# Kernel tuning notes

Hardware: AMD Instinct MI355X
Metric: run time of the kernel (lower is better)

Reference implementation:

```python
import jax, jax.numpy as jnp
import numpy as np


def _log_g(x):
    # log_g(x) = log(relu(x)+1) if x >= 0 else x
    return jnp.where(x >= 0, jnp.log1p(jnp.maximum(x, 0.0)), x)


def _min_gru(hg):
    # hg: [B, H, L] -> [B, H/2, L]
    h, gate = jnp.split(hg, 2, axis=1)
    log_coeffs = -jax.nn.softplus(gate)                    # log(1 - z)
    log_values = -jax.nn.softplus(-gate) + _log_g(h)       # log(z) + log g(h)
    a_star = jnp.cumsum(log_coeffs, axis=2)
    log_h0_plus_b_star = jax.lax.cumlogsumexp(log_values - a_star, axis=2)
    return jnp.exp(a_star + log_h0_plus_b_star)


def setup_inputs() -> dict:
    key = jax.random.key(0)
    B, H, L = 8, 512, 8192
    x = jax.random.normal(key, (B, H, L), dtype=jnp.float32)
    return {"x": x}


def reference(x) -> jnp.ndarray:
    # bidirectional minGRU: forward scan on first half of channels,
    # reversed scan on second half.
    fore, back = jnp.split(x, 2, axis=1)
    out_fore = _min_gru(fore)
    out_back = jnp.flip(_min_gru(jnp.flip(back, axis=2)), axis=2)
    return jnp.concatenate([out_fore, out_back], axis=1)  # [B, H/2, L]
```

## Files before the change

kernel.cpp:

```cpp
#include <hip/hip_runtime.h>
#include <math.h>


#define SEQ_L 8192
#define NTHREADS 256
#define PER_THREAD 8
#define TILE (NTHREADS * PER_THREAD)
#define NTILES (SEQ_L / TILE)

__global__ __launch_bounds__(NTHREADS) void mingru_scan_kernel(
    const float* __restrict__ x, float* __restrict__ out) {
    const int blk = blockIdx.x;
    const int dir = blk >> 10;
    const int s   = blk & 1023;
    const int b   = s >> 7;
    const int c   = s & 127;

    const int tid  = threadIdx.x;
    const int lane = tid & 63;
    const int wave = tid >> 6;

    const float* __restrict__ hrow = x + (size_t)((b * 512) + (dir * 256) + c) * SEQ_L;
    const float* __restrict__ grow = hrow + (size_t)128 * SEQ_L;
    float* __restrict__ orow = out + (size_t)((b * 256) + (dir * 128) + c) * SEQ_L;

    __shared__ float sA[2][4];
    __shared__ float sB[2][4];

    float carry = 0.0f;

    {
    }
    int base0 = tid * PER_THREAD;
    int idx0  = dir ? (SEQ_L - base0 - PER_THREAD) : base0;
    float4 nh0 = *(const float4*)(hrow + idx0);
    float4 nh1 = *(const float4*)(hrow + idx0 + 4);
    float4 ng0 = *(const float4*)(grow + idx0);
    float4 ng1 = *(const float4*)(grow + idx0 + 4);

#pragma unroll
    for (int t = 0; t < NTILES; ++t) {
        const float4 h0 = nh0, h1 = nh1, g0 = ng0, g1 = ng1;

        if (t + 1 < NTILES) {
            const int nb = (t + 1) * TILE + tid * PER_THREAD;
            const int ni = dir ? (SEQ_L - nb - PER_THREAD) : nb;
            nh0 = *(const float4*)(hrow + ni);
            nh1 = *(const float4*)(hrow + ni + 4);
            ng0 = *(const float4*)(grow + ni);
            ng1 = *(const float4*)(grow + ni + 4);
        }

        float hv[PER_THREAD], gv[PER_THREAD];
        if (dir == 0) {
            hv[0]=h0.x; hv[1]=h0.y; hv[2]=h0.z; hv[3]=h0.w;
            hv[4]=h1.x; hv[5]=h1.y; hv[6]=h1.z; hv[7]=h1.w;
            gv[0]=g0.x; gv[1]=g0.y; gv[2]=g0.z; gv[3]=g0.w;
            gv[4]=g1.x; gv[5]=g1.y; gv[6]=g1.z; gv[7]=g1.w;
        } else {
            hv[0]=h1.w; hv[1]=h1.z; hv[2]=h1.y; hv[3]=h1.x;
            hv[4]=h0.w; hv[5]=h0.z; hv[6]=h0.y; hv[7]=h0.x;
            gv[0]=g1.w; gv[1]=g1.z; gv[2]=g1.y; gv[3]=g1.x;
            gv[4]=g0.w; gv[5]=g0.z; gv[6]=g0.y; gv[7]=g0.x;
        }

        float pp[PER_THREAD], ov0[PER_THREAD];
        float ca = 1.0f, cb = 0.0f;
#pragma unroll
        for (int j = 0; j < PER_THREAD; ++j) {
            const float gt = gv[j];
            const float e  = __expf(-fabsf(gt));
            const float r  = 1.0f / (1.0f + e);
            const float sn = e * r;
            const float z  = (gt >= 0.0f) ? r  : sn;
            const float a  = (gt >= 0.0f) ? sn : r;
            const float hh = hv[j];
            const float gf = (hh >= 0.0f) ? (hh + 1.0f) : __expf(hh);
            const float bb = z * gf;
            cb = a * cb + bb;
            ca = a * ca;
            ov0[j] = cb;
            pp[j]  = ca;
        }

        float pa = ca, pb = cb;
#pragma unroll
        for (int d = 1; d < 64; d <<= 1) {
            const float oa = __shfl_up(pa, d);
            const float ob = __shfl_up(pb, d);
            if (lane >= d) {
                pb = pa * ob + pb;
                pa = pa * oa;
            }
        }

        const int buf = t & 1;
        if (lane == 63) { sA[buf][wave] = pa; sB[buf][wave] = pb; }
        __syncthreads();

        float st = carry;
        for (int w = 0; w < wave; ++w) st = sA[buf][w] * st + sB[buf][w];
        float ea = __shfl_up(pa, 1);
        float eb = __shfl_up(pb, 1);
        if (lane == 0) { ea = 1.0f; eb = 0.0f; }
        st = ea * st + eb;

        float ov[PER_THREAD];
#pragma unroll
        for (int j = 0; j < PER_THREAD; ++j) ov[j] = ov0[j] + st * pp[j];

        const int base = t * TILE + tid * PER_THREAD;
        if (dir == 0) {
            *(float4*)(orow + base)     = make_float4(ov[0], ov[1], ov[2], ov[3]);
            *(float4*)(orow + base + 4) = make_float4(ov[4], ov[5], ov[6], ov[7]);
        } else {
            const int p = SEQ_L - base - PER_THREAD;
            *(float4*)(orow + p)     = make_float4(ov[7], ov[6], ov[5], ov[4]);
            *(float4*)(orow + p + 4) = make_float4(ov[3], ov[2], ov[1], ov[0]);
        }

        float nc = carry;
#pragma unroll
        for (int w = 0; w < 4; ++w) nc = sA[buf][w] * nc + sB[buf][w];
        carry = nc;
    }
}

extern "C" void kernel_launch(void* const* d_in, const int* in_sizes, int n_in,
                              void* d_out, int out_size, void* d_ws, size_t ws_size,
                              hipStream_t stream) {
    const float* x = (const float*)d_in[0];
    float* out = (float*)d_out;
    mingru_scan_kernel<<<2048, NTHREADS, 0, stream>>>(x, out);
}
```

Measured before the change: 209.5 us.

## Scan whole row in one pass with 1024-thread blocks and nontemporal memory ops

Each block now uses 1024 threads so a full 8192-element row is handled in a single tile, with no loop over four tiles and no carry chain between them. The cross-wave combine now reads 16 wave aggregates from shared memory using a predicated unrolled loop. Loads and stores become nontemporal vector accesses to avoid polluting cache with streamed data. In exchange, occupancy now depends on register use at 1024 threads per block, and the load prefetching across tiles is gone, so latency is covered only by running many waves at once.

```diff
diff --git a/kernel.cpp b/kernel.cpp
--- a/kernel.cpp
+++ b/kernel.cpp
@@ -3,12 +3,12 @@
 
 
 #define SEQ_L 8192
-#define NTHREADS 256
+#define NTHREADS 1024
 #define PER_THREAD 8
-#define TILE (NTHREADS * PER_THREAD)
-#define NTILES (SEQ_L / TILE)
 
-__global__ __launch_bounds__(NTHREADS) void mingru_scan_kernel(
+typedef float f4 __attribute__((ext_vector_type(4)));
+
+__global__ __launch_bounds__(NTHREADS, 8) void mingru_scan_kernel(
     const float* __restrict__ x, float* __restrict__ out) {
     const int blk = blockIdx.x;
     const int dir = blk >> 10;
@@ -24,105 +24,90 @@
     const float* __restrict__ grow = hrow + (size_t)128 * SEQ_L;
     float* __restrict__ orow = out + (size_t)((b * 256) + (dir * 128) + c) * SEQ_L;
 
-    __shared__ float sA[2][4];
-    __shared__ float sB[2][4];
+    __shared__ float sA[16];
+    __shared__ float sB[16];
 
-    float carry = 0.0f;
+    const int base = tid * PER_THREAD;
+    const int idx  = dir ? (SEQ_L - base - PER_THREAD) : base;
 
-    {
+    const f4 h0 = __builtin_nontemporal_load((const f4*)(hrow + idx));
+    const f4 h1 = __builtin_nontemporal_load((const f4*)(hrow + idx + 4));
+    const f4 g0 = __builtin_nontemporal_load((const f4*)(grow + idx));
+    const f4 g1 = __builtin_nontemporal_load((const f4*)(grow + idx + 4));
+
+    float hv[PER_THREAD], gv[PER_THREAD];
+    if (dir == 0) {
+        hv[0]=h0.x; hv[1]=h0.y; hv[2]=h0.z; hv[3]=h0.w;
+        hv[4]=h1.x; hv[5]=h1.y; hv[6]=h1.z; hv[7]=h1.w;
+        gv[0]=g0.x; gv[1]=g0.y; gv[2]=g0.z; gv[3]=g0.w;
+        gv[4]=g1.x; gv[5]=g1.y; gv[6]=g1.z; gv[7]=g1.w;
+    } else {
+        hv[0]=h1.w; hv[1]=h1.z; hv[2]=h1.y; hv[3]=h1.x;
+        hv[4]=h0.w; hv[5]=h0.z; hv[6]=h0.y; hv[7]=h0.x;
+        gv[0]=g1.w; gv[1]=g1.z; gv[2]=g1.y; gv[3]=g1.x;
+        gv[4]=g0.w; gv[5]=g0.z; gv[6]=g0.y; gv[7]=g0.x;
     }
-    int base0 = tid * PER_THREAD;
-    int idx0  = dir ? (SEQ_L - base0 - PER_THREAD) : base0;
-    float4 nh0 = *(const float4*)(hrow + idx0);
-    float4 nh1 = *(const float4*)(hrow + idx0 + 4);
-    float4 ng0 = *(const float4*)(grow + idx0);
-    float4 ng1 = *(const float4*)(grow + idx0 + 4);
 
+    float pp[PER_THREAD], ov0[PER_THREAD];
+    float ca = 1.0f, cb = 0.0f;
 #pragma unroll
-    for (int t = 0; t < NTILES; ++t) {
-        const float4 h0 = nh0, h1 = nh1, g0 = ng0, g1 = ng1;
+    for (int j = 0; j < PER_THREAD; ++j) {
+        const float gt = gv[j];
+        const float e  = __expf(-fabsf(gt));
+        const float r  = 1.0f / (1.0f + e);
+        const float sn = e * r;
+        const float z  = (gt >= 0.0f) ? r  : sn;
+        const float a  = (gt >= 0.0f) ? sn : r;
+        const float hh = hv[j];
+        const float gf = (hh >= 0.0f) ? (hh + 1.0f) : __expf(hh);
+        const float bb = z * gf;
+        cb = a * cb + bb;
+        ca = a * ca;
+        ov0[j] = cb;
+        pp[j]  = ca;
+    }
 
-        if (t + 1 < NTILES) {
-            const int nb = (t + 1) * TILE + tid * PER_THREAD;
-            const int ni = dir ? (SEQ_L - nb - PER_THREAD) : nb;
-            nh0 = *(const float4*)(hrow + ni);
-            nh1 = *(const float4*)(hrow + ni + 4);
-            ng0 = *(const float4*)(grow + ni);
-            ng1 = *(const float4*)(grow + ni + 4);
+    float pa = ca, pb = cb;
+#pragma unroll
+    for (int d = 1; d < 64; d <<= 1) {
+        const float oa = __shfl_up(pa, d);
+        const float ob = __shfl_up(pb, d);
+        if (lane >= d) {
+            pb = pa * ob + pb;
+            pa = pa * oa;
         }
+    }
 
-        float hv[PER_THREAD], gv[PER_THREAD];
-        if (dir == 0) {
-            hv[0]=h0.x; hv[1]=h0.y; hv[2]=h0.z; hv[3]=h0.w;
-            hv[4]=h1.x; hv[5]=h1.y; hv[6]=h1.z; hv[7]=h1.w;
-            gv[0]=g0.x; gv[1]=g0.y; gv[2]=g0.z; gv[3]=g0.w;
-            gv[4]=g1.x; gv[5]=g1.y; gv[6]=g1.z; gv[7]=g1.w;
-        } else {
-            hv[0]=h1.w; hv[1]=h1.z; hv[2]=h1.y; hv[3]=h1.x;
-            hv[4]=h0.w; hv[5]=h0.z; hv[6]=h0.y; hv[7]=h0.x;
-            gv[0]=g1.w; gv[1]=g1.z; gv[2]=g1.y; gv[3]=g1.x;
-            gv[4]=g0.w; gv[5]=g0.z; gv[6]=g0.y; gv[7]=g0.x;
-        }
+    if (lane == 63) { sA[wave] = pa; sB[wave] = pb; }
+    __syncthreads();
 
-        float pp[PER_THREAD], ov0[PER_THREAD];
-        float ca = 1.0f, cb = 0.0f;
+    float st = 0.0f;
 #pragma unroll
-        for (int j = 0; j < PER_THREAD; ++j) {
-            const float gt = gv[j];
-            const float e  = __expf(-fabsf(gt));
-            const float r  = 1.0f / (1.0f + e);
-            const float sn = e * r;
-            const float z  = (gt >= 0.0f) ? r  : sn;
-            const float a  = (gt >= 0.0f) ? sn : r;
-            const float hh = hv[j];
-            const float gf = (hh >= 0.0f) ? (hh + 1.0f) : __expf(hh);
-            const float bb = z * gf;
-            cb = a * cb + bb;
-            ca = a * ca;
-            ov0[j] = cb;
-            pp[j]  = ca;
-        }
+    for (int w = 0; w < 15; ++w) {
+        const float aw = sA[w];
+        const float bw = sB[w];
+        if (w < wave) st = aw * st + bw;
+    }
 
-        float pa = ca, pb = cb;
+    float ea = __shfl_up(pa, 1);
+    float eb = __shfl_up(pb, 1);
+    if (lane == 0) { ea = 1.0f; eb = 0.0f; }
+    st = ea * st + eb;
+
+    float ov[PER_THREAD];
 #pragma unroll
-        for (int d = 1; d < 64; d <<= 1) {
-            const float oa = __shfl_up(pa, d);
-            const float ob = __shfl_up(pb, d);
-            if (lane >= d) {
-                pb = pa * ob + pb;
-                pa = pa * oa;
-            }
-        }
+    for (int j = 0; j < PER_THREAD; ++j) ov[j] = ov0[j] + st * pp[j];
 
-        const int buf = t & 1;
-        if (lane == 63) { sA[buf][wave] = pa; sB[buf][wave] = pb; }
-        __syncthreads();
-
-        float st = carry;
-        for (int w = 0; w < wave; ++w) st = sA[buf][w] * st + sB[buf][w];
-        float ea = __shfl_up(pa, 1);
-        float eb = __shfl_up(pb, 1);
-        if (lane == 0) { ea = 1.0f; eb = 0.0f; }
-        st = ea * st + eb;
-
-        float ov[PER_THREAD];
-#pragma unroll
-        for (int j = 0; j < PER_THREAD; ++j) ov[j] = ov0[j] + st * pp[j];
-
-        const int base = t * TILE + tid * PER_THREAD;
-        if (dir == 0) {
-            *(float4*)(orow + base)     = make_float4(ov[0], ov[1], ov[2], ov[3]);
-            *(float4*)(orow + base + 4) = make_float4(ov[4], ov[5], ov[6], ov[7]);
-        } else {
-            const int p = SEQ_L - base - PER_THREAD;
-            *(float4*)(orow + p)     = make_float4(ov[7], ov[6], ov[5], ov[4]);
-            *(float4*)(orow + p + 4) = make_float4(ov[3], ov[2], ov[1], ov[0]);
-        }
-
-        float nc = carry;
-#pragma unroll
-        for (int w = 0; w < 4; ++w) nc = sA[buf][w] * nc + sB[buf][w];
-        carry = nc;
+    if (dir == 0) {
+        f4 o0; o0.x = ov[0]; o0.y = ov[1]; o0.z = ov[2]; o0.w = ov[3];
+        f4 o1; o1.x = ov[4]; o1.y = ov[5]; o1.z = ov[6]; o1.w = ov[7];
+        __builtin_nontemporal_store(o0, (f4*)(orow + base));
+        __builtin_nontemporal_store(o1, (f4*)(orow + base + 4));
+    } else {
+        f4 o0; o0.x = ov[7]; o0.y = ov[6]; o0.z = ov[5]; o0.w = ov[4];
+        f4 o1; o1.x = ov[3]; o1.y = ov[2]; o1.z = ov[1]; o1.w = ov[0];
+        __builtin_nontemporal_store(o0, (f4*)(orow + idx));
+        __builtin_nontemporal_store(o1, (f4*)(orow + idx + 4));
     }
 }
 
```

Result: faster. 201.2 us, median of 2 (-4.0%).
